# Optimization experiments

Measured on AMD Instinct MI355X. Metric: run time of the kernel, lower is better.

The kernel has to match this reference:

```python
import jax, jax.numpy as jnp
import numpy as np
import math

B, S, H, D = 2, 2048, 12, 64
DIM = H * D
TOTAL = B * S


def setup_inputs() -> dict:
    key = jax.random.key(0)
    ks = jax.random.split(key, 5)
    hidden_states = jax.random.normal(ks[0], (TOTAL, DIM), dtype=jnp.float32)
    Wqkv_w = jax.random.normal(ks[1], (3 * DIM, DIM), dtype=jnp.float32) * (1.0 / math.sqrt(DIM))
    Wqkv_b = jax.random.normal(ks[2], (3 * DIM,), dtype=jnp.float32) * 0.02
    bias = jax.random.normal(ks[3], (B, H, S, S), dtype=jnp.float32) * 0.1
    slopes = jax.random.uniform(ks[4], (H,), dtype=jnp.float32)
    cu_seqlens = jnp.array([0, S, 2 * S], dtype=jnp.int32)
    indices = jnp.arange(TOTAL, dtype=jnp.int64)
    attn_mask = jnp.ones((B, S), dtype=jnp.int32)
    return {"hidden_states": hidden_states, "Wqkv_w": Wqkv_w, "Wqkv_b": Wqkv_b,
            "bias": bias, "slopes": slopes, "cu_seqlens": cu_seqlens,
            "indices": indices, "attn_mask": attn_mask, "max_seqlen": S}


def reference(hidden_states, Wqkv_w, Wqkv_b, bias, slopes, cu_seqlens, indices, attn_mask, max_seqlen):
    total_nnz, dim = hidden_states.shape
    batch = cu_seqlens.shape[0] - 1
    # fused QKV projection (torch Linear: x @ W.T + b)
    qkv = hidden_states @ Wqkv_w.T + Wqkv_b  # (total_nnz, 3*dim)
    # pad_input: scatter unpadded rows into (batch*max_seqlen, 3*dim)
    padded = jnp.zeros((batch * max_seqlen, 3 * dim), dtype=qkv.dtype).at[indices].set(qkv)
    qkv = padded.reshape(batch, max_seqlen, 3, H, D)
    q = qkv[:, :, 0].transpose(0, 2, 1, 3)  # (b, h, s, d)
    k = qkv[:, :, 1].transpose(0, 2, 1, 3)
    v = qkv[:, :, 2].transpose(0, 2, 1, 3)
    scores = jnp.einsum('bhqd,bhkd->bhqk', q, k) / math.sqrt(D)
    scores = scores + bias  # ALiBi (dense bias tensor)
    probs = jax.nn.softmax(scores, axis=-1)  # dropout p=0 -> identity
    attn = jnp.einsum('bhqk,bhkd->bhqd', probs, v)
    attn = attn.transpose(0, 2, 1, 3).reshape(batch * max_seqlen, dim)
    # unpad_input_only: gather valid rows back
    return attn[indices]
```

## Files before the change

### kernel.cpp

```cpp
#include <hip/hip_runtime.h>


typedef __attribute__((ext_vector_type(8))) short short8;
typedef __attribute__((ext_vector_type(4))) float floatx4;
typedef unsigned short u16;
typedef unsigned int u32;

#define LOG2E 1.4426950408889634f

__device__ __forceinline__ u16 f2bf(float f) {
  u32 u = __float_as_uint(f);
  u += 0x7FFFu + ((u >> 16) & 1u);
  return (u16)(u >> 16);
}

typedef const __attribute__((address_space(1))) u32* gp_t;
typedef __attribute__((address_space(3))) u32* lp_t;
__device__ __forceinline__ void async_cp16(const void* g, void* l) {
  __builtin_amdgcn_global_load_lds((gp_t)g, (lp_t)l, 16, 0, 0);
}

__global__ __launch_bounds__(256) void pack_kernel(
    const float* __restrict__ A, const float* __restrict__ W,
    u16* __restrict__ Abf, u16* __restrict__ Wbf) {
  unsigned u = blockIdx.x * 256u + threadIdx.x;
  const unsigned nA = 786432u;
  float4 v;
  u16* dst;
  if (u < nA) { v = ((const float4*)A)[u]; dst = Abf + u * 4; }
  else        { unsigned q = u - nA; v = ((const float4*)W)[q]; dst = Wbf + q * 4; }
  ushort4 o;
  o.x = f2bf(v.x); o.y = f2bf(v.y); o.z = f2bf(v.z); o.w = f2bf(v.w);
  *(ushort4*)dst = o;
}

__global__ __launch_bounds__(256, 2) void qkv_gemm(
    const u16* __restrict__ Abf, const u16* __restrict__ Wbf,
    const float* __restrict__ bq,
    u16* __restrict__ Qb, u16* __restrict__ Kb, u16* __restrict__ Vb) {
  __shared__ __align__(16) char smem[16384];
  char* As = smem;
  char* Bs = smem + 8192;
  const unsigned t = threadIdx.x;
  const unsigned nblk = blockIdx.x, mblk = blockIdx.y;
  const unsigned w = t >> 6, l = t & 63, quad = l >> 4, c = l & 15;
  const unsigned wm = (w >> 1) * 64, wn = (w & 1) * 64;

  floatx4 acc[4][4] = {};

  const unsigned b0 = t, b1 = t + 256u;
  const unsigned r0 = b0 >> 2, ch0 = (b0 & 3u) ^ (r0 & 3u);
  const unsigned r1 = b1 >> 2, ch1 = (b1 & 3u) ^ (r1 & 3u);
  const char* gA0 = (const char*)Abf + (size_t)((mblk * 128 + r0) * 768) * 2 + ch0 * 16;
  const char* gA1 = (const char*)Abf + (size_t)((mblk * 128 + r1) * 768) * 2 + ch1 * 16;
  const char* gB0 = (const char*)Wbf + (size_t)((nblk * 128 + r0) * 768) * 2 + ch0 * 16;
  const char* gB1 = (const char*)Wbf + (size_t)((nblk * 128 + r1) * 768) * 2 + ch1 * 16;

  for (unsigned kt = 0; kt < 24; ++kt) {
    __syncthreads();
    async_cp16(gA0 + kt * 64, As + b0 * 16);
    async_cp16(gA1 + kt * 64, As + b1 * 16);
    async_cp16(gB0 + kt * 64, Bs + b0 * 16);
    async_cp16(gB1 + kt * 64, Bs + b1 * 16);
    __syncthreads();
    short8 af[4], bf[4];
#pragma unroll
    for (int mt = 0; mt < 4; ++mt) {
      unsigned row = wm + mt * 16 + c;
      af[mt] = *(const short8*)(As + row * 64 + 16 * (quad ^ (row & 3u)));
    }
#pragma unroll
    for (int nt = 0; nt < 4; ++nt) {
      unsigned row = wn + nt * 16 + c;
      bf[nt] = *(const short8*)(Bs + row * 64 + 16 * (quad ^ (row & 3u)));
    }
#pragma unroll
    for (int mt = 0; mt < 4; ++mt)
#pragma unroll
      for (int nt = 0; nt < 4; ++nt)
        acc[mt][nt] = __builtin_amdgcn_mfma_f32_16x16x32_bf16(af[mt], bf[nt], acc[mt][nt], 0, 0, 0);
  }

  float bqv[4];
#pragma unroll
  for (int nt = 0; nt < 4; ++nt) bqv[nt] = bq[nblk * 128 + wn + nt * 16 + c];
#pragma unroll
  for (int mt = 0; mt < 4; ++mt) {
#pragma unroll
    for (int r = 0; r < 4; ++r) {
      unsigned m = mblk * 128 + wm + mt * 16 + quad * 4 + r;
      unsigned bb = m >> 11, s = m & 2047u;
#pragma unroll
      for (int nt = 0; nt < 4; ++nt) {
        float val = acc[mt][nt][r] + bqv[nt];
        unsigned n = nblk * 128 + wn + nt * 16 + c;
        u16 bv = f2bf(val);
        if (n < 768u) {
          unsigned h = n >> 6, d = n & 63u;
          Qb[(((bb * 12 + h) * 2048 + s) << 6) + d] = bv;
        } else if (n < 1536u) {
          unsigned n2 = n - 768u, h = n2 >> 6, d = n2 & 63u;
          Kb[(((bb * 12 + h) * 2048 + s) << 6) + d] = bv;
        } else {
          unsigned n2 = n - 1536u, h = n2 >> 6, d = n2 & 63u;
          Vb[(((bb * 12 + h) << 6) + d) * 2048 + s] = bv;
        }
      }
    }
  }
}

__global__ __launch_bounds__(256, 3) void attn_kernel(
    const u16* __restrict__ Qb, const u16* __restrict__ Kb,
    const u16* __restrict__ Vb, const float* __restrict__ bias,
    float* __restrict__ out) {
  __shared__ __align__(16) char smem[32768];
  char* Qs = smem;
  char* Ks = smem + 8192;
  char* Vs = smem + 16384;
  char* Ps = smem + 24576;
  const unsigned t = threadIdx.x;
  const unsigned bh = blockIdx.x >> 5, qt = blockIdx.x & 31u;
  const unsigned q0 = qt * 64;
  const unsigned w = t >> 6, l = t & 63, quad = l >> 4, c = l & 15;

  const unsigned b0 = t, b1 = t + 256u;
  const unsigned r0 = b0 >> 3, ch0 = (b0 & 7u) ^ (r0 & 7u);
  const unsigned r1 = b1 >> 3, ch1 = (b1 & 7u) ^ (r1 & 7u);

  async_cp16((const char*)Qb + (size_t)(bh * 2048 + q0 + r0) * 128 + ch0 * 16, Qs + b0 * 16);
  async_cp16((const char*)Qb + (size_t)(bh * 2048 + q0 + r1) * 128 + ch1 * 16, Qs + b1 * 16);
  __syncthreads();
  short8 aq[2];
  {
    unsigned row = w * 16 + c;
    aq[0] = *(const short8*)(Qs + row * 128 + 16 * ((quad + 0u) ^ (row & 7u)));
    aq[1] = *(const short8*)(Qs + row * 128 + 16 * ((quad + 4u) ^ (row & 7u)));
  }

  float mrun[4] = {-1e30f, -1e30f, -1e30f, -1e30f};
  float lrun[4] = {0.f, 0.f, 0.f, 0.f};
  floatx4 oacc[4] = {};

  const char* gK0 = (const char*)Kb + (size_t)(bh * 2048 + r0) * 128 + ch0 * 16;
  const char* gK1 = (const char*)Kb + (size_t)(bh * 2048 + r1) * 128 + ch1 * 16;
  const char* gV0 = (const char*)Vb + (size_t)(bh * 64 + r0) * 4096 + ch0 * 16;
  const char* gV1 = (const char*)Vb + (size_t)(bh * 64 + r1) * 4096 + ch1 * 16;
  const float* bias_base = bias + (size_t)(bh * 2048 + q0 + w * 16 + quad * 4) * 2048 + c;
  const unsigned pb = w * 2048u;

  for (unsigned k0 = 0; k0 < 2048; k0 += 64) {
    __syncthreads();
    async_cp16(gK0 + (size_t)k0 * 128, Ks + b0 * 16);
    async_cp16(gK1 + (size_t)k0 * 128, Ks + b1 * 16);
    async_cp16(gV0 + (size_t)k0 * 2, Vs + b0 * 16);
    async_cp16(gV1 + (size_t)k0 * 2, Vs + b1 * 16);
    __syncthreads();

    float bv[4][4];
#pragma unroll
    for (int tt = 0; tt < 4; ++tt)
#pragma unroll
      for (int r = 0; r < 4; ++r)
        bv[tt][r] = bias_base[(size_t)r * 2048 + k0 + tt * 16];

    floatx4 s4[4] = {};
#pragma unroll
    for (int ds = 0; ds < 2; ++ds)
#pragma unroll
      for (int tt = 0; tt < 4; ++tt) {
        unsigned row = tt * 16 + c;
        short8 kf = *(const short8*)(Ks + row * 128 + 16 * (((unsigned)quad + 4u * ds) ^ (c & 7u)));
        s4[tt] = __builtin_amdgcn_mfma_f32_16x16x32_bf16(aq[ds], kf, s4[tt], 0, 0, 0);
      }

    float alpha[4];
    float pr[4][4];
#pragma unroll
    for (int r = 0; r < 4; ++r) {
      float x0 = fmaf(bv[0][r], 8.0f, s4[0][r]) * (LOG2E / 8.0f);
      float x1 = fmaf(bv[1][r], 8.0f, s4[1][r]) * (LOG2E / 8.0f);
      float x2 = fmaf(bv[2][r], 8.0f, s4[2][r]) * (LOG2E / 8.0f);
      float x3 = fmaf(bv[3][r], 8.0f, s4[3][r]) * (LOG2E / 8.0f);
      float mx = fmaxf(fmaxf(x0, x1), fmaxf(x2, x3));
      mx = fmaxf(mx, __shfl_xor(mx, 1));
      mx = fmaxf(mx, __shfl_xor(mx, 2));
      mx = fmaxf(mx, __shfl_xor(mx, 4));
      mx = fmaxf(mx, __shfl_xor(mx, 8));
      float mn = fmaxf(mrun[r], mx);
      float a = __builtin_amdgcn_exp2f(mrun[r] - mn);
      mrun[r] = mn;
      float p0 = __builtin_amdgcn_exp2f(x0 - mn);
      float p1 = __builtin_amdgcn_exp2f(x1 - mn);
      float p2 = __builtin_amdgcn_exp2f(x2 - mn);
      float p3 = __builtin_amdgcn_exp2f(x3 - mn);
      pr[0][r] = p0; pr[1][r] = p1; pr[2][r] = p2; pr[3][r] = p3;
      float rs = (p0 + p1) + (p2 + p3);
      rs += __shfl_xor(rs, 1);
      rs += __shfl_xor(rs, 2);
      rs += __shfl_xor(rs, 4);
      rs += __shfl_xor(rs, 8);
      lrun[r] = lrun[r] * a + rs;
      alpha[r] = a;
    }
#pragma unroll
    for (int dt = 0; dt < 4; ++dt) {
      oacc[dt][0] *= alpha[0]; oacc[dt][1] *= alpha[1];
      oacc[dt][2] *= alpha[2]; oacc[dt][3] *= alpha[3];
    }

#pragma unroll
    for (int tt = 0; tt < 4; ++tt)
#pragma unroll
      for (int r = 0; r < 4; ++r) {
        unsigned qq = quad * 4 + r;
        unsigned off = pb + qq * 128 + 16 * (((unsigned)(2 * tt) + (c >> 3)) ^ (qq & 7u)) + 2 * (c & 7u);
        *(u16*)(Ps + off) = f2bf(pr[tt][r]);
      }
    asm volatile("s_waitcnt lgkmcnt(0)" ::: "memory");

#pragma unroll
    for (int js = 0; js < 2; ++js) {
      short8 pf = *(const short8*)(Ps + pb + (l & 15) * 128 +
                                   16 * (((unsigned)quad + 4u * js) ^ ((l & 15) & 7u)));
#pragma unroll
      for (int dt = 0; dt < 4; ++dt) {
        unsigned row = dt * 16 + c;
        short8 vf = *(const short8*)(Vs + row * 128 + 16 * (((unsigned)quad + 4u * js) ^ (c & 7u)));
        oacc[dt] = __builtin_amdgcn_mfma_f32_16x16x32_bf16(pf, vf, oacc[dt], 0, 0, 0);
      }
    }
  }

  unsigned b_ = bh / 12u, h = bh % 12u;
#pragma unroll
  for (int r = 0; r < 4; ++r) {
    float li = 1.0f / lrun[r];
    unsigned qg = q0 + w * 16 + quad * 4 + r;
    float* op = out + (size_t)(b_ * 2048 + qg) * 768 + h * 64 + c;
#pragma unroll
    for (int dt = 0; dt < 4; ++dt) op[dt * 16] = oacc[dt][r] * li;
  }
}

extern "C" void kernel_launch(void* const* d_in, const int* in_sizes, int n_in,
                              void* d_out, int out_size, void* d_ws, size_t ws_size,
                              hipStream_t stream) {
  const float* hidden = (const float*)d_in[0];
  const float* Wqkv_w = (const float*)d_in[1];
  const float* Wqkv_b = (const float*)d_in[2];
  const float* bias   = (const float*)d_in[3];
  float* out = (float*)d_out;

  char* ws = (char*)d_ws;
  u16* Abf = (u16*)(ws);
  u16* Wbf = (u16*)(ws + 6291456);
  u16* Qb  = (u16*)(ws + 9830400);
  u16* Kb  = (u16*)(ws + 16121856);
  u16* Vb  = (u16*)(ws + 22413312);

  pack_kernel<<<4800, 256, 0, stream>>>(hidden, Wqkv_w, Abf, Wbf);
  qkv_gemm<<<dim3(18, 32), 256, 0, stream>>>(Abf, Wbf, Wqkv_b, Qb, Kb, Vb);
  attn_kernel<<<768, 256, 0, stream>>>(Qb, Kb, Vb, bias, out);
}
```

Measured before the change: 600.8 us.

## Double-buffer LDS tiles in QKV GEMM and attention, prefetch bias, swizzle block order

```diff
diff --git a/kernel.cpp b/kernel.cpp
--- a/kernel.cpp
+++ b/kernel.cpp
@@ -34,15 +34,19 @@
   *(ushort4*)dst = o;
 }
 
-__global__ __launch_bounds__(256, 2) void qkv_gemm(
+__global__ __launch_bounds__(256, 3) void qkv_gemm(
     const u16* __restrict__ Abf, const u16* __restrict__ Wbf,
     const float* __restrict__ bq,
     u16* __restrict__ Qb, u16* __restrict__ Kb, u16* __restrict__ Vb) {
-  __shared__ __align__(16) char smem[16384];
-  char* As = smem;
-  char* Bs = smem + 8192;
+  __shared__ __align__(16) char smem[32768];
+  char* As0 = smem;
+  char* Bs0 = smem + 8192;
+  char* As1 = smem + 16384;
+  char* Bs1 = smem + 24576;
   const unsigned t = threadIdx.x;
-  const unsigned nblk = blockIdx.x, mblk = blockIdx.y;
+  unsigned orig = blockIdx.y * 18u + blockIdx.x;
+  unsigned wg = (orig & 7u) * 72u + (orig >> 3);
+  const unsigned nblk = wg % 18u, mblk = wg / 18u;
   const unsigned w = t >> 6, l = t & 63, quad = l >> 4, c = l & 15;
   const unsigned wm = (w >> 1) * 64, wn = (w & 1) * 64;
 
@@ -56,29 +60,40 @@
   const char* gB0 = (const char*)Wbf + (size_t)((nblk * 128 + r0) * 768) * 2 + ch0 * 16;
   const char* gB1 = (const char*)Wbf + (size_t)((nblk * 128 + r1) * 768) * 2 + ch1 * 16;
 
+  async_cp16(gA0, As0 + b0 * 16);
+  async_cp16(gA1, As0 + b1 * 16);
+  async_cp16(gB0, Bs0 + b0 * 16);
+  async_cp16(gB1, Bs0 + b1 * 16);
+  __syncthreads();
+
   for (unsigned kt = 0; kt < 24; ++kt) {
-    __syncthreads();
-    async_cp16(gA0 + kt * 64, As + b0 * 16);
-    async_cp16(gA1 + kt * 64, As + b1 * 16);
-    async_cp16(gB0 + kt * 64, Bs + b0 * 16);
-    async_cp16(gB1 + kt * 64, Bs + b1 * 16);
-    __syncthreads();
+    char* Ac = (kt & 1u) ? As1 : As0;
+    char* Bc = (kt & 1u) ? Bs1 : Bs0;
+    if (kt + 1 < 24) {
+      char* An = (kt & 1u) ? As0 : As1;
+      char* Bn = (kt & 1u) ? Bs0 : Bs1;
+      async_cp16(gA0 + (kt + 1) * 64, An + b0 * 16);
+      async_cp16(gA1 + (kt + 1) * 64, An + b1 * 16);
+      async_cp16(gB0 + (kt + 1) * 64, Bn + b0 * 16);
+      async_cp16(gB1 + (kt + 1) * 64, Bn + b1 * 16);
+    }
     short8 af[4], bf[4];
 #pragma unroll
     for (int mt = 0; mt < 4; ++mt) {
       unsigned row = wm + mt * 16 + c;
-      af[mt] = *(const short8*)(As + row * 64 + 16 * (quad ^ (row & 3u)));
+      af[mt] = *(const short8*)(Ac + row * 64 + 16 * (quad ^ (row & 3u)));
     }
 #pragma unroll
     for (int nt = 0; nt < 4; ++nt) {
       unsigned row = wn + nt * 16 + c;
-      bf[nt] = *(const short8*)(Bs + row * 64 + 16 * (quad ^ (row & 3u)));
+      bf[nt] = *(const short8*)(Bc + row * 64 + 16 * (quad ^ (row & 3u)));
     }
 #pragma unroll
     for (int mt = 0; mt < 4; ++mt)
 #pragma unroll
       for (int nt = 0; nt < 4; ++nt)
         acc[mt][nt] = __builtin_amdgcn_mfma_f32_16x16x32_bf16(af[mt], bf[nt], acc[mt][nt], 0, 0, 0);
+    __syncthreads();
   }
 
   float bqv[4];
@@ -114,33 +129,22 @@
     const u16* __restrict__ Qb, const u16* __restrict__ Kb,
     const u16* __restrict__ Vb, const float* __restrict__ bias,
     float* __restrict__ out) {
-  __shared__ __align__(16) char smem[32768];
-  char* Qs = smem;
-  char* Ks = smem + 8192;
-  char* Vs = smem + 16384;
-  char* Ps = smem + 24576;
+  __shared__ __align__(16) char smem[49152];
+  char* Qs  = smem;
+  char* Ks0 = smem + 8192;
+  char* Ks1 = smem + 16384;
+  char* Vs0 = smem + 24576;
+  char* Vs1 = smem + 32768;
+  char* Ps  = smem + 40960;
   const unsigned t = threadIdx.x;
-  const unsigned bh = blockIdx.x >> 5, qt = blockIdx.x & 31u;
+  unsigned wgid = (blockIdx.x & 7u) * 96u + (blockIdx.x >> 3);
+  const unsigned bh = wgid >> 5, qt = wgid & 31u;
   const unsigned q0 = qt * 64;
   const unsigned w = t >> 6, l = t & 63, quad = l >> 4, c = l & 15;
 
   const unsigned b0 = t, b1 = t + 256u;
   const unsigned r0 = b0 >> 3, ch0 = (b0 & 7u) ^ (r0 & 7u);
   const unsigned r1 = b1 >> 3, ch1 = (b1 & 7u) ^ (r1 & 7u);
-
-  async_cp16((const char*)Qb + (size_t)(bh * 2048 + q0 + r0) * 128 + ch0 * 16, Qs + b0 * 16);
-  async_cp16((const char*)Qb + (size_t)(bh * 2048 + q0 + r1) * 128 + ch1 * 16, Qs + b1 * 16);
-  __syncthreads();
-  short8 aq[2];
-  {
-    unsigned row = w * 16 + c;
-    aq[0] = *(const short8*)(Qs + row * 128 + 16 * ((quad + 0u) ^ (row & 7u)));
-    aq[1] = *(const short8*)(Qs + row * 128 + 16 * ((quad + 4u) ^ (row & 7u)));
-  }
-
-  float mrun[4] = {-1e30f, -1e30f, -1e30f, -1e30f};
-  float lrun[4] = {0.f, 0.f, 0.f, 0.f};
-  floatx4 oacc[4] = {};
 
   const char* gK0 = (const char*)Kb + (size_t)(bh * 2048 + r0) * 128 + ch0 * 16;
   const char* gK1 = (const char*)Kb + (size_t)(bh * 2048 + r1) * 128 + ch1 * 16;
@@ -149,39 +153,70 @@
   const float* bias_base = bias + (size_t)(bh * 2048 + q0 + w * 16 + quad * 4) * 2048 + c;
   const unsigned pb = w * 2048u;
 
-  for (unsigned k0 = 0; k0 < 2048; k0 += 64) {
-    __syncthreads();
-    async_cp16(gK0 + (size_t)k0 * 128, Ks + b0 * 16);
-    async_cp16(gK1 + (size_t)k0 * 128, Ks + b1 * 16);
-    async_cp16(gV0 + (size_t)k0 * 2, Vs + b0 * 16);
-    async_cp16(gV1 + (size_t)k0 * 2, Vs + b1 * 16);
-    __syncthreads();
-
-    float bv[4][4];
-#pragma unroll
-    for (int tt = 0; tt < 4; ++tt)
-#pragma unroll
-      for (int r = 0; r < 4; ++r)
-        bv[tt][r] = bias_base[(size_t)r * 2048 + k0 + tt * 16];
+  async_cp16((const char*)Qb + (size_t)(bh * 2048 + q0 + r0) * 128 + ch0 * 16, Qs + b0 * 16);
+  async_cp16((const char*)Qb + (size_t)(bh * 2048 + q0 + r1) * 128 + ch1 * 16, Qs + b1 * 16);
+  async_cp16(gK0, Ks0 + b0 * 16);
+  async_cp16(gK1, Ks0 + b1 * 16);
+  async_cp16(gV0, Vs0 + b0 * 16);
+  async_cp16(gV1, Vs0 + b1 * 16);
+  float bvA[4][4], bvB[4][4];
+#pragma unroll
+  for (int tt = 0; tt < 4; ++tt)
+#pragma unroll
+    for (int r = 0; r < 4; ++r)
+      bvA[tt][r] = bias_base[(size_t)r * 2048 + tt * 16];
+  __syncthreads();
+
+  short8 aq[2];
+  {
+    unsigned row = w * 16 + c;
+    aq[0] = *(const short8*)(Qs + row * 128 + 16 * ((quad + 0u) ^ (row & 7u)));
+    aq[1] = *(const short8*)(Qs + row * 128 + 16 * ((quad + 4u) ^ (row & 7u)));
+  }
+
+  float mrun[4] = {-1e30f, -1e30f, -1e30f, -1e30f};
+  float lrun[4] = {0.f, 0.f, 0.f, 0.f};
+  floatx4 oacc[4] = {};
+
+  for (unsigned tix = 0; tix < 32; ++tix) {
+    const unsigned k0 = tix * 64u;
+    const char* Kc = (tix & 1u) ? Ks1 : Ks0;
+    const char* Vc = (tix & 1u) ? Vs1 : Vs0;
+
+    if (tix + 1 < 32) {
+      char* Kn = (tix & 1u) ? Ks0 : Ks1;
+      char* Vn = (tix & 1u) ? Vs0 : Vs1;
+      async_cp16(gK0 + (size_t)(k0 + 64) * 128, Kn + b0 * 16);
+      async_cp16(gK1 + (size_t)(k0 + 64) * 128, Kn + b1 * 16);
+      async_cp16(gV0 + (size_t)(k0 + 64) * 2, Vn + b0 * 16);
+      async_cp16(gV1 + (size_t)(k0 + 64) * 2, Vn + b1 * 16);
+#pragma unroll
+      for (int tt = 0; tt < 4; ++tt)
+#pragma unroll
+        for (int r = 0; r < 4; ++r)
+          bvB[tt][r] = bias_base[(size_t)r * 2048 + (k0 + 64) + tt * 16];
+    }
 
     floatx4 s4[4] = {};
+    __builtin_amdgcn_s_setprio(1);
 #pragma unroll
     for (int ds = 0; ds < 2; ++ds)
 #pragma unroll
       for (int tt = 0; tt < 4; ++tt) {
         unsigned row = tt * 16 + c;
-        short8 kf = *(const short8*)(Ks + row * 128 + 16 * (((unsigned)quad + 4u * ds) ^ (c & 7u)));
+        short8 kf = *(const short8*)(Kc + row * 128 + 16 * (((unsigned)quad + 4u * ds) ^ (c & 7u)));
         s4[tt] = __builtin_amdgcn_mfma_f32_16x16x32_bf16(aq[ds], kf, s4[tt], 0, 0, 0);
       }
+    __builtin_amdgcn_s_setprio(0);
 
     float alpha[4];
     float pr[4][4];
 #pragma unroll
     for (int r = 0; r < 4; ++r) {
-      float x0 = fmaf(bv[0][r], 8.0f, s4[0][r]) * (LOG2E / 8.0f);
-      float x1 = fmaf(bv[1][r], 8.0f, s4[1][r]) * (LOG2E / 8.0f);
-      float x2 = fmaf(bv[2][r], 8.0f, s4[2][r]) * (LOG2E / 8.0f);
-      float x3 = fmaf(bv[3][r], 8.0f, s4[3][r]) * (LOG2E / 8.0f);
+      float x0 = fmaf(bvA[0][r], 8.0f, s4[0][r]) * (LOG2E / 8.0f);
+      float x1 = fmaf(bvA[1][r], 8.0f, s4[1][r]) * (LOG2E / 8.0f);
+      float x2 = fmaf(bvA[2][r], 8.0f, s4[2][r]) * (LOG2E / 8.0f);
+      float x3 = fmaf(bvA[3][r], 8.0f, s4[3][r]) * (LOG2E / 8.0f);
       float mx = fmaxf(fmaxf(x0, x1), fmaxf(x2, x3));
       mx = fmaxf(mx, __shfl_xor(mx, 1));
       mx = fmaxf(mx, __shfl_xor(mx, 2));
@@ -219,6 +254,7 @@
       }
     asm volatile("s_waitcnt lgkmcnt(0)" ::: "memory");
 
+    __builtin_amdgcn_s_setprio(1);
 #pragma unroll
     for (int js = 0; js < 2; ++js) {
       short8 pf = *(const short8*)(Ps + pb + (l & 15) * 128 +
@@ -226,9 +262,20 @@
 #pragma unroll
       for (int dt = 0; dt < 4; ++dt) {
         unsigned row = dt * 16 + c;
-        short8 vf = *(const short8*)(Vs + row * 128 + 16 * (((unsigned)quad + 4u * js) ^ (c & 7u)));
+        short8 vf = *(const short8*)(Vc + row * 128 + 16 * (((unsigned)quad + 4u * js) ^ (c & 7u)));
         oacc[dt] = __builtin_amdgcn_mfma_f32_16x16x32_bf16(pf, vf, oacc[dt], 0, 0, 0);
       }
+    }
+    __builtin_amdgcn_s_setprio(0);
+
+    __syncthreads();
+
+    if (tix + 1 < 32) {
+#pragma unroll
+      for (int tt = 0; tt < 4; ++tt)
+#pragma unroll
+        for (int r = 0; r < 4; ++r)
+          bvA[tt][r] = bvB[tt][r];
     }
   }
 
```

Result: no change. 599.2 us (-0.3%).
